# Kernel tuning notes

Measured on AMD Instinct MI355X. Metric: run time of the kernel, lower is better.

## Reference

```python
import jax, jax.numpy as jnp
import numpy as np

KS, KT = 3, 3  # Chebyshev order, temporal kernel


def _conv_t(x, w, b):
    # x: [B,C,T,N], w: [C_out,C_in,KT,1] -> valid conv over T
    y = jax.lax.conv_general_dilated(x, w, (1, 1), 'VALID',
                                     dimension_numbers=('NCHW', 'OIHW', 'NCHW'))
    return y + b[None, :, None, None]


def _glu_tconv(x, w, b, aw, ab):
    c_out = w.shape[0] // 2
    # Align (c_in > c_out): 1x1 conv, then crop first KT-1 steps
    x_in = (jnp.einsum('bctn,oc->botn', x, aw) + ab[None, :, None, None])[:, :, KT - 1:, :]
    xc = _conv_t(x, w, b)
    return (xc[:, :c_out] + x_in) * jax.nn.sigmoid(xc[:, c_out:])


def _relu_tconv(x, w, b):
    c_out = w.shape[0]
    pad = c_out - x.shape[1]
    # Align (c_in < c_out): zero-pad channels, then crop first KT-1 steps
    x_in = jnp.pad(x, ((0, 0), (0, pad), (0, 0), (0, 0)))[:, :, KT - 1:, :]
    return jax.nn.relu(_conv_t(x, w, b) + x_in)


def _sconv(x, basis, theta, bias):
    # Chebyshev graph conv: knm,bitm -> bitkn then channel mix iok,bitkn -> botn
    x_c = jnp.einsum('knm,bitm->bitkn', basis, x)
    x_gc = jnp.einsum('iok,bitkn->botn', theta, x_c) + bias[None, :, None, None]
    return jax.nn.relu(x_gc + x)  # align is identity (c_in == c_out)


def _layer_norm(x, g, b):
    # LayerNorm over [node_num, channels]: permute to [B,T,N,C], normalize last 2 dims
    y = jnp.transpose(x, (0, 2, 3, 1))
    mu = jnp.mean(y, axis=(-2, -1), keepdims=True)
    var = jnp.var(y, axis=(-2, -1), keepdims=True)
    y = (y - mu) * jax.lax.rsqrt(var + 1e-5) * g + b
    return jnp.transpose(y, (0, 3, 1, 2))


def _cheb_basis(graph):
    n = graph.shape[0]
    eye = jnp.eye(n, dtype=graph.dtype)
    g = graph + eye
    d = jnp.clip(jnp.sum(g, axis=-1), 1e-6, None) ** -0.5
    lap = eye - d[:, None] * g * d[None, :]
    cheb = [eye, lap]
    for _ in range(2, KS):
        cheb.append(2.0 * (lap @ cheb[-1]) - cheb[-2])
    return jnp.stack(cheb[:KS])


def _block(x, basis, t1_w, t1_b, t1_aw, t1_ab, s_theta, s_bias, t2_w, t2_b, ln_g, ln_b):
    x = _glu_tconv(x, t1_w, t1_b, t1_aw, t1_ab)
    x = _sconv(x, basis, s_theta, s_bias)
    x = _relu_tconv(x, t2_w, t2_b)
    return _layer_norm(x, ln_g, ln_b)  # dropout: eval mode (identity)


def setup_inputs() -> dict:
    B, N, T = 16, 2000, 12
    D_IN, D_OUT, C_MID = 3, 64, 32
    keys = jax.random.split(jax.random.key(0), 24)
    k = iter(range(24))

    def nrm(shape, scale=0.05):
        return jax.random.normal(keys[next(k)], shape, dtype=jnp.float32) * scale

    inp = {}
    inp['x'] = jax.random.normal(keys[next(k)], (B, D_IN, T, N), dtype=jnp.float32)
    inp['graph'] = jax.random.uniform(keys[next(k)], (N, N), dtype=jnp.float32)
    inp['in_w'] = nrm((D_IN, D_OUT), 0.3)
    inp['in_b'] = nrm((D_OUT,))
    for blk in ('b1', 'b2'):
        inp[blk + '_t1_w'] = nrm((2 * C_MID, D_OUT, KT, 1))
        inp[blk + '_t1_b'] = nrm((2 * C_MID,))
        inp[blk + '_t1_aw'] = nrm((C_MID, D_OUT))
        inp[blk + '_t1_ab'] = nrm((C_MID,))
        inp[blk + '_s_theta'] = nrm((C_MID, C_MID, KS))
        inp[blk + '_s_bias'] = nrm((C_MID,))
        inp[blk + '_t2_w'] = nrm((D_OUT, C_MID, KT, 1))
        inp[blk + '_t2_b'] = nrm((D_OUT,))
        inp[blk + '_ln_g'] = jnp.ones((N, D_OUT), dtype=jnp.float32)
        inp[blk + '_ln_b'] = jnp.zeros((N, D_OUT), dtype=jnp.float32)
    return inp


def reference(x, graph, in_w, in_b,
              b1_t1_w, b1_t1_b, b1_t1_aw, b1_t1_ab, b1_s_theta, b1_s_bias,
              b1_t2_w, b1_t2_b, b1_ln_g, b1_ln_b,
              b2_t1_w, b2_t1_b, b2_t1_aw, b2_t1_ab, b2_s_theta, b2_s_bias,
              b2_t2_w, b2_t2_b, b2_ln_g, b2_ln_b):
    # input_conv: 1x1 conv == channel matmul
    h = jnp.einsum('bctn,co->botn', x, in_w) + in_b[None, :, None, None]
    basis = _cheb_basis(graph)
    h = _block(h, basis, b1_t1_w, b1_t1_b, b1_t1_aw, b1_t1_ab,
               b1_s_theta, b1_s_bias, b1_t2_w, b1_t2_b, b1_ln_g, b1_ln_b)
    h = _block(h, basis, b2_t1_w, b2_t1_b, b2_t1_aw, b2_t1_ab,
               b2_s_theta, b2_s_bias, b2_t2_w, b2_t2_b, b2_ln_g, b2_ln_b)
    return h  # [B, 64, T-4*(KT-1)=4, N]
```

## Files before the change

### kernel.cpp

```cpp
#include <hip/hip_runtime.h>


typedef unsigned short u16;
typedef __attribute__((ext_vector_type(8))) short short8;
typedef __attribute__((ext_vector_type(4))) float floatx4;

struct __attribute__((aligned(8))) us4 { u16 v[4]; };

#define AS1 __attribute__((address_space(1)))
#define AS3 __attribute__((address_space(3)))

__device__ __forceinline__ float b2f(u16 h) {
  union { unsigned int u; float f; } v;
  v.u = ((unsigned int)h) << 16;
  return v.f;
}
__device__ __forceinline__ u16 f2b(float f) {
  union { float f; unsigned int u; } v;
  v.f = f;
  unsigned int r = (v.u + 0x7fffu + ((v.u >> 16) & 1u)) >> 16;
  return (u16)r;
}
__device__ __forceinline__ void gl_lds16(const u16* g, u16* l) {
  __builtin_amdgcn_global_load_lds((const AS1 unsigned int*)g,
                                   (AS3 unsigned int*)l, 16, 0, 0);
}
__device__ __forceinline__ us4 load4_guard(const u16* gp, int n) {
  if (n + 3 < 2000) return *(const us4*)gp;
  us4 r;
#pragma unroll
  for (int i = 0; i < 4; ++i) r.v[i] = (n + i < 2000) ? gp[i] : (u16)0;
  return r;
}


__global__ void k_deg(const float* __restrict__ graph, float* __restrict__ d) {
  const int n = blockIdx.x;
  const int tid = threadIdx.x;
  float s = 0.f;
  const float* row = graph + (size_t)n * 2000;
  for (int m4 = tid; m4 < 500; m4 += 256) {
    const float4 g = *(const float4*)(row + m4 * 4);
    s += (g.x + g.y) + (g.z + g.w);
  }
  __shared__ float red[256];
  red[tid] = s;
  __syncthreads();
  for (int st = 128; st > 0; st >>= 1) {
    if (tid < st) red[tid] += red[tid + st];
    __syncthreads();
  }
  if (tid == 0) d[n] = rsqrtf(fmaxf(red[0] + 1.f, 1e-6f));
}

__global__ void k_lap(const float* __restrict__ graph, const float* __restrict__ d,
                      u16* __restrict__ L) {
  const int m = blockIdx.x * 1024 + threadIdx.x * 4;
  const int n = blockIdx.y;
  us4 r = {{0, 0, 0, 0}};
  if (n < 2000 && m < 2000) {
    const float4 g4 = *(const float4*)(graph + (size_t)n * 2000 + m);
    const float4 d4 = *(const float4*)(d + m);
    const float dn = d[n];
    const float gv[4] = {g4.x, g4.y, g4.z, g4.w};
    const float dv[4] = {d4.x, d4.y, d4.z, d4.w};
#pragma unroll
    for (int i = 0; i < 4; ++i) {
      const float delta = (n == m + i) ? 1.f : 0.f;
      r.v[i] = f2b(delta - dn * (gv[i] + delta) * dv[i]);
    }
  }
  *(us4*)(L + (size_t)n * 2048 + m) = r;
}

__global__ __launch_bounds__(256, 4)
void k_inconv(const float* __restrict__ x, const float* __restrict__ w,
              const float* __restrict__ bias, u16* __restrict__ h0T) {
  const int n0 = blockIdx.x * 64;
  const int b = blockIdx.y / 12, t = blockIdx.y % 12;
  const int tid = threadIdx.x;
  u16* outb = h0T + ((size_t)(b * 12 + t) * 2048 + n0) * 64;
  const float* xb = x + ((size_t)(b * 3) * 12 + t) * 2000;
#pragma unroll
  for (int q = 0; q < 4; ++q) {
    const int f = q * 256 + tid;
    const int nl = f >> 4;
    const int c4 = (f & 15) * 4;
    const int n = n0 + nl;
    us4 r = {{0, 0, 0, 0}};
    if (n < 2000) {
      const float a0 = xb[n];
      const float a1 = xb[12 * 2000 + n];
      const float a2 = xb[2 * 12 * 2000 + n];
#pragma unroll
      for (int j = 0; j < 4; ++j) {
        const int o = c4 + j;
        r.v[j] = f2b(a0 * w[o] + a1 * w[64 + o] + a2 * w[128 + o] + bias[o]);
      }
    }
    *(us4*)(outb + f * 4) = r;
  }
}

__global__ void k_wpack(const float* __restrict__ t1w, const float* __restrict__ aw,
                        const float* __restrict__ th, const float* __restrict__ t2w,
                        u16* __restrict__ wglu, u16* __restrict__ wth,
                        u16* __restrict__ wt2) {
  const int mode = blockIdx.x;
  const int tid = threadIdx.x;
  if (mode == 0) {
    for (int idx = tid; idx < 1536 * 8; idx += 256) {
      int chunk = idx >> 3, j = idx & 7;
      int l15 = chunk & 15, quad = (chunk >> 4) & 3, g = chunk >> 6;
      int ks = g % 6, mi = g / 6;
      int o = mi * 16 + l15;
      int k = ks * 32 + quad * 8 + j;
      int c = k & 63, dt = k >> 6;
      float v = t1w[(o * 64 + c) * 3 + dt];
      if (o < 32 && dt == 2) v += aw[o * 64 + c];
      wglu[idx] = f2b(v);
    }
  } else if (mode == 1) {
    for (int idx = tid; idx < 512 * 8; idx += 256) {
      int chunk = idx >> 3, j = idx & 7;
      int l15 = chunk & 15, quad = (chunk >> 4) & 3, g = chunk >> 6;
      float v = 0.f;
      if (g < 6) {
        int ks = g % 3, mi = g / 3;
        int o = mi * 16 + l15;
        int k = ks * 32 + quad * 8 + j;
        int i = k & 31, src = k >> 5;
        const float* p = th + (i * 32 + o) * 3;
        v = (src == 0) ? (p[0] - p[2]) : (src == 1 ? p[1] : 2.f * p[2]);
      }
      wth[idx] = f2b(v);
    }
  } else {
    for (int idx = tid; idx < 768 * 8; idx += 256) {
      int chunk = idx >> 3, j = idx & 7;
      int l15 = chunk & 15, quad = (chunk >> 4) & 3, g = chunk >> 6;
      int ks = g % 3, mi = g / 3;
      int o = mi * 16 + l15;
      int k = ks * 32 + quad * 8 + j;
      int i = k & 31, dt = k >> 5;
      wt2[idx] = f2b(t2w[(o * 32 + i) * 3 + dt]);
    }
  }
}

__global__ __launch_bounds__(256, 4)
void k_mixT(const u16* __restrict__ xT, const u16* __restrict__ wp,
            const float* __restrict__ b0, const float* __restrict__ b1,
            u16* __restrict__ out, int T_in, int T, int tcnt) {
  __shared__ __align__(16) u16 lw[1536 * 8];
  __shared__ __align__(16) u16 lo[2][32][72];
  const int tid = threadIdx.x;
  const int lane = tid & 63, wave = tid >> 6;
  const int quad = lane >> 4, l15 = lane & 15;
  const int n0 = blockIdx.x * 64;
  const int b = blockIdx.y;
  const int t0 = blockIdx.z * tcnt;

#pragma unroll
  for (int p = 0; p < 6; ++p)
    gl_lds16(wp + (size_t)(p * 256 + wave * 64 + lane) * 8,
             &lw[(p * 256 + wave * 64) * 8]);

  float svb[8], gtb[8];
#pragma unroll
  for (int mi = 0; mi < 2; ++mi)
#pragma unroll
    for (int r = 0; r < 4; ++r) {
      const int i = mi * 16 + quad * 4 + r;
      svb[mi * 4 + r] = b0[i] + b1[i];
      gtb[mi * 4 + r] = b0[32 + i];
    }

  const int n = n0 + wave * 16 + l15;
  const size_t PL = (size_t)2048 * 64;
  const u16* px = xT + ((size_t)(b * T_in + t0) * 2048 + n) * 64 + quad * 8;

  short8 fa = *(const short8*)(px);
  short8 fb = *(const short8*)(px + 32);
  short8 fc = *(const short8*)(px + PL);
  short8 fd = *(const short8*)(px + PL + 32);

  const int rch = tid >> 3;
  const int rn8 = (tid & 7) * 8;

  asm volatile("s_waitcnt vmcnt(0)" ::: "memory");
  __syncthreads();

  for (int tt = 0; tt < tcnt; ++tt) {
    const int t = t0 + tt;
    const short8 fe = *(const short8*)(px + 2 * PL);
    const short8 ff = *(const short8*)(px + 2 * PL + 32);
    px += PL;

    floatx4 acc[4] = {};
    const short8 fr[6] = {fa, fb, fc, fd, fe, ff};
#pragma unroll
    for (int ks = 0; ks < 6; ++ks)
#pragma unroll
      for (int mi = 0; mi < 4; ++mi) {
        short8 afr = *(const short8*)&lw[((mi * 6 + ks) * 64 + lane) * 8];
        acc[mi] = __builtin_amdgcn_mfma_f32_16x16x32_bf16(afr, fr[ks], acc[mi], 0, 0, 0);
      }
    fa = fc; fb = fd; fc = fe; fd = ff;

    u16(*lob)[72] = lo[tt & 1];
#pragma unroll
    for (int mi = 0; mi < 2; ++mi)
#pragma unroll
      for (int r = 0; r < 4; ++r) {
        const int i = mi * 16 + quad * 4 + r;
        const float sv = acc[mi][r] + svb[mi * 4 + r];
        const float gt = acc[mi + 2][r] + gtb[mi * 4 + r];
        const float val = sv / (1.f + __expf(-gt));
        lob[i][wave * 16 + l15] = f2b(val);
      }
    __syncthreads();

    *(short8*)(out + (size_t)((b * 32 + rch) * T + t) * 2048 + n0 + rn8) =
        *(const short8*)&lob[rch][rn8];
  }
}

__global__ __launch_bounds__(256, 2)
void k_mix12(const u16* __restrict__ x0, const u16* __restrict__ y1,
             const u16* __restrict__ y2, const u16* __restrict__ wth,
             const u16* __restrict__ wt2, const float* __restrict__ sb,
             const float* __restrict__ t2b, u16* __restrict__ out,
             int T_g, int T_o) {
  __shared__ __align__(16) u16 lw1[512 * 8];
  __shared__ __align__(16) u16 lw2[768 * 8];
  __shared__ __align__(16) u16 lx[780 * 8];
  __shared__ __align__(16) u16 lt[10 * 260 * 8];

  const int tid = threadIdx.x;
  const int lane = tid & 63, wave = tid >> 6;
  const int quad = lane >> 4, l15 = lane & 15;
  const int n0 = blockIdx.x * 64;
  const int b = blockIdx.y;
  const int n = n0 + wave * 16 + l15;

#pragma unroll
  for (int p = 0; p < 2; ++p)
    gl_lds16(wth + (size_t)(p * 256 + wave * 64 + lane) * 8,
             &lw1[(p * 256 + wave * 64) * 8]);
#pragma unroll
  for (int p = 0; p < 3; ++p)
    gl_lds16(wt2 + (size_t)(p * 256 + wave * 64 + lane) * 8,
             &lw2[(p * 256 + wave * 64) * 8]);

  const int nloc = (tid & 15) * 4;
  const int g16 = tid >> 4;

  for (int t = 0; t < T_g; ++t) {
    __syncthreads();
    us4 rv[2][4];
#pragma unroll
    for (int p = 0; p < 2; ++p) {
      const int k4 = p * 16 + g16;
      if (k4 < 24) {
#pragma unroll
        for (int i = 0; i < 4; ++i) {
          const int k = k4 * 4 + i;
          const u16* base = (k < 32) ? x0 : ((k < 64) ? y1 : y2);
          rv[p][i] = *(const us4*)(base +
              (size_t)((b * 32 + (k & 31)) * T_g + t) * 2048 + n0 + nloc);
        }
      }
    }
#pragma unroll
    for (int p = 0; p < 2; ++p) {
      const int k4 = p * 16 + g16;
      if (k4 < 24) {
        const int ks = k4 >> 3, q8 = k4 & 7;
        const int quadw = (q8 >> 1) & 3;
        const int j0 = (q8 & 1) * 4;
#pragma unroll
        for (int i = 0; i < 4; ++i) {
          const int nn = nloc + i;
          const int chunk = (ks * 4 + (nn >> 4)) * 65 + quadw * 16 + (nn & 15);
          us4 wv;
          wv.v[0] = rv[p][0].v[i]; wv.v[1] = rv[p][1].v[i];
          wv.v[2] = rv[p][2].v[i]; wv.v[3] = rv[p][3].v[i];
          *(us4*)&lx[chunk * 8 + j0] = wv;
        }
      }
    }
    __syncthreads();

    floatx4 acc[2] = {};
#pragma unroll
    for (int ks = 0; ks < 3; ++ks) {
      short8 bfr = *(const short8*)&lx[((ks * 4 + wave) * 65 + lane) * 8];
#pragma unroll
      for (int mi = 0; mi < 2; ++mi) {
        short8 afr = *(const short8*)&lw1[((mi * 3 + ks) * 64 + lane) * 8];
        acc[mi] = __builtin_amdgcn_mfma_f32_16x16x32_bf16(afr, bfr, acc[mi], 0, 0, 0);
      }
    }
#pragma unroll
    for (int mi = 0; mi < 2; ++mi)
#pragma unroll
      for (int r = 0; r < 4; ++r) {
        const int o = mi * 16 + quad * 4 + r;
        const float v = acc[mi][r] + sb[o] +
            b2f(lx[(wave * 65 + ((o >> 3) & 3) * 16 + l15) * 8 + (o & 7)]);
        lt[((t * 4 + wave) * 65 + ((o >> 3) & 3) * 16 + l15) * 8 + (o & 7)] =
            f2b(fmaxf(v, 0.f));
      }
  }
  __syncthreads();

  for (int to = 0; to < T_o; ++to) {
    floatx4 acc[4] = {};
#pragma unroll
    for (int ks = 0; ks < 3; ++ks) {
      short8 bfr = *(const short8*)&lt[(((to + ks) * 4 + wave) * 65 + lane) * 8];
#pragma unroll
      for (int mi = 0; mi < 4; ++mi) {
        short8 afr = *(const short8*)&lw2[((mi * 3 + ks) * 64 + lane) * 8];
        acc[mi] = __builtin_amdgcn_mfma_f32_16x16x32_bf16(afr, bfr, acc[mi], 0, 0, 0);
      }
    }
    if (n < 2000) {
#pragma unroll
      for (int mi = 0; mi < 4; ++mi)
#pragma unroll
        for (int r = 0; r < 4; ++r) {
          const int o = mi * 16 + quad * 4 + r;
          float v = acc[mi][r] + t2b[o];
          if (o < 32)
            v += b2f(lt[(((to + 2) * 4 + wave) * 65 +
                         ((o >> 3) & 3) * 16 + l15) * 8 + (o & 7)]);
          out[(size_t)((b * 64 + o) * T_o + to) * 2000 + n] = f2b(fmaxf(v, 0.f));
        }
    }
  }
}

template <int BM, int MPAD, int DPW>
__global__ __launch_bounds__(512, 1)
void k_gemm(const u16* __restrict__ A, const u16* __restrict__ Bt,
            u16* __restrict__ C) {
  constexpr int K = 2048;
  constexpr int NTI = K / 64;
  constexpr int AFR = BM / 32;
  constexpr int WM = BM / 2;
  constexpr int S1 = (AFR + 1) / 2;
  constexpr int C1 = DPW - 4;
  constexpr int BROWS = 512;
  constexpr int ROWS = BROWS + 2 * MPAD;
  __shared__ __align__(16) u16 lds[2][ROWS * 32];

  const int tid = threadIdx.x;
  const int lane = tid & 63, wave = tid >> 6;
  const int quad = lane >> 4, l15 = lane & 15;
  const int m0 = blockIdx.y * BM, n0 = blockIdx.x * 256;
  const int wy = wave >> 2, wx = wave & 3;

  const int lr = lane >> 2;
  const int qv = (((lane & 3) - (lr + (lr >> 2))) & 3);
  const u16* sp[DPW];
  int dofs[DPW];
#pragma unroll
  for (int d = 0; d < DPW; ++d) {
    const int f = wave * DPW + d;
    if (f < 32) {
      const int rb = f >> 1, ks = f & 1;
      sp[d] = Bt + (size_t)(n0 + rb * 16 + lr) * K + ks * 32 + qv * 8;
      dofs[d] = (ks * 256 + rb * 16) * 32;
    } else {
      const int g = f - 32;
      const int rb = g >> 1, ks = g & 1;
      sp[d] = A + (size_t)(m0 + rb * 16 + lr) * K + ks * 32 + qv * 8;
      dofs[d] = (BROWS + ks * MPAD + rb * 16) * 32;
    }
  }

  const int sigr = (l15 + (l15 >> 2)) & 3;
  const int cofs = ((quad + sigr) & 3) * 8;

  floatx4 acc[AFR][4] = {};

#pragma unroll
  for (int d = 0; d < DPW; ++d) gl_lds16(sp[d], &lds[0][dofs[d]]);
#pragma unroll
  for (int d = 0; d < C1; ++d) gl_lds16(sp[d] + 64, &lds[1][dofs[d]]);
  if constexpr (C1 == 3) asm volatile("s_waitcnt vmcnt(3)" ::: "memory");
  else                   asm volatile("s_waitcnt vmcnt(2)" ::: "memory");
  asm volatile("s_barrier" ::: "memory");

  for (int it = 0; it < NTI; ++it) {
    const u16* cb = lds[it & 1];
    u16* nb = lds[(it & 1) ^ 1];
    u16* pb = lds[it & 1];
    const int kn1 = (it + 1) * 64;
    const bool st1 = (it + 1 < NTI);
    short8 bf[4], af[AFR];

#pragma unroll
    for (int ni = 0; ni < 4; ++ni)
      bf[ni] = *(const short8*)&cb[(wx * 64 + ni * 16 + l15) * 32 + cofs];
#pragma unroll
    for (int mi = 0; mi < S1; ++mi)
      af[mi] = *(const short8*)&cb[(BROWS + wy * WM + mi * 16 + l15) * 32 + cofs];
    if (st1) {
      gl_lds16(sp[C1] + kn1, &nb[dofs[C1]]);
      gl_lds16(sp[C1 + 1] + kn1, &nb[dofs[C1 + 1]]);
    }
#pragma unroll
    for (int mi = 0; mi < S1; ++mi)
#pragma unroll
      for (int ni = 0; ni < 4; ++ni)
        acc[mi][ni] = __builtin_amdgcn_mfma_f32_16x16x32_bf16(
            af[mi], bf[ni], acc[mi][ni], 0, 0, 0);

#pragma unroll
    for (int mi = S1; mi < AFR; ++mi)
      af[mi] = *(const short8*)&cb[(BROWS + wy * WM + mi * 16 + l15) * 32 + cofs];
    if (st1) {
      gl_lds16(sp[C1 + 2] + kn1, &nb[dofs[C1 + 2]]);
      gl_lds16(sp[C1 + 3] + kn1, &nb[dofs[C1 + 3]]);
    }
#pragma unroll
    for (int mi = S1; mi < AFR; ++mi)
#pragma unroll
      for (int ni = 0; ni < 4; ++ni)
        acc[mi][ni] = __builtin_amdgcn_mfma_f32_16x16x32_bf16(
            af[mi], bf[ni], acc[mi][ni], 0, 0, 0);

#pragma unroll
    for (int ni = 0; ni < 4; ++ni)
      bf[ni] = *(const short8*)&cb[(256 + wx * 64 + ni * 16 + l15) * 32 + cofs];
#pragma unroll
    for (int mi = 0; mi < S1; ++mi)
      af[mi] = *(const short8*)&cb[(BROWS + MPAD + wy * WM + mi * 16 + l15) * 32 + cofs];
#pragma unroll
    for (int mi = 0; mi < S1; ++mi)
#pragma unroll
      for (int ni = 0; ni < 4; ++ni)
        acc[mi][ni] = __builtin_amdgcn_mfma_f32_16x16x32_bf16(
            af[mi], bf[ni], acc[mi][ni], 0, 0, 0);

#pragma unroll
    for (int mi = S1; mi < AFR; ++mi)
      af[mi] = *(const short8*)&cb[(BROWS + MPAD + wy * WM + mi * 16 + l15) * 32 + cofs];
#pragma unroll
    for (int mi = S1; mi < AFR; ++mi)
#pragma unroll
      for (int ni = 0; ni < 4; ++ni)
        acc[mi][ni] = __builtin_amdgcn_mfma_f32_16x16x32_bf16(
            af[mi], bf[ni], acc[mi][ni], 0, 0, 0);

    asm volatile("s_waitcnt lgkmcnt(0)" ::: "memory");
    asm volatile("s_barrier" ::: "memory");
    if (it + 2 < NTI) {
      const int kn2 = (it + 2) * 64;
#pragma unroll
      for (int d = 0; d < C1; ++d) gl_lds16(sp[d] + kn2, &pb[dofs[d]]);
      if constexpr (C1 == 3) asm volatile("s_waitcnt vmcnt(3)" ::: "memory");
      else                   asm volatile("s_waitcnt vmcnt(2)" ::: "memory");
    } else {
      asm volatile("s_waitcnt vmcnt(0)" ::: "memory");
    }
    asm volatile("s_barrier" ::: "memory");
  }

#pragma unroll
  for (int mi = 0; mi < AFR; ++mi) {
#pragma unroll
    for (int ni = 0; ni < 4; ++ni) {
      const int row = m0 + wy * WM + mi * 16 + quad * 4;
      const int col = n0 + wx * 64 + ni * 16 + l15;
#pragma unroll
      for (int r = 0; r < 4; ++r)
        C[(size_t)(row + r) * K + col] = f2b(acc[mi][ni][r]);
    }
  }
}


__global__ void k_lnpart(const u16* __restrict__ h, float* __restrict__ part, int T) {
  const int bt = blockIdx.x, cg = blockIdx.y;
  const int b = bt / T, t = bt % T;
  const int tid = threadIdx.x;
  float s = 0.f, ss = 0.f;
  for (int c = cg * 8; c < cg * 8 + 8; ++c) {
    const u16* row = h + (size_t)((b * 64 + c) * T + t) * 2000;
    for (int n = tid * 4; n < 2000; n += 1024) {
      const us4 hv = *(const us4*)(row + n);
#pragma unroll
      for (int i = 0; i < 4; ++i) {
        const float v = b2f(hv.v[i]);
        s += v; ss += v * v;
      }
    }
  }
  __shared__ float r1[256], r2[256];
  r1[tid] = s; r2[tid] = ss;
  __syncthreads();
  for (int st = 128; st > 0; st >>= 1) {
    if (tid < st) { r1[tid] += r1[tid + st]; r2[tid] += r2[tid + st]; }
    __syncthreads();
  }
  if (tid == 0) {
    part[(bt * 8 + cg) * 2 + 0] = r1[0];
    part[(bt * 8 + cg) * 2 + 1] = r2[0];
  }
}

__global__ void k_lnfin(const float* __restrict__ part, float* __restrict__ stats,
                        int BT) {
  const int i = blockIdx.x * 256 + threadIdx.x;
  if (i >= BT) return;
  float s = 0.f, ss = 0.f;
  for (int g = 0; g < 8; ++g) {
    s  += part[(i * 8 + g) * 2 + 0];
    ss += part[(i * 8 + g) * 2 + 1];
  }
  const float inv = 1.f / 128000.f;
  const float mu = s * inv;
  const float var = ss * inv - mu * mu;
  stats[i * 2] = mu;
  stats[i * 2 + 1] = rsqrtf(var + 1e-5f);
}

__global__ __launch_bounds__(256, 4)
void k_lnapT(const u16* __restrict__ h, const float* __restrict__ stats,
             const float* __restrict__ gw, const float* __restrict__ gb,
             u16* __restrict__ hT, int T) {
  __shared__ u16 tile[64][72];
  const int tid = threadIdx.x;
  const int n0 = blockIdx.x * 64;
  const int bt = blockIdx.y;
  const int b = bt / T, t = bt % T;
  const float mu = stats[bt * 2], rs = stats[bt * 2 + 1];

  {
    const int c = tid >> 2;
    const int nq = (tid & 3) * 16;
    const u16* row = h + (size_t)((b * 64 + c) * T + t) * 2000 + n0 + nq;
#pragma unroll
    for (int k = 0; k < 4; ++k) {
      const us4 v = load4_guard(row + k * 4, n0 + nq + k * 4);
      *(us4*)&tile[c][nq + k * 4] = v;
    }
  }
  __syncthreads();

  const int n = tid >> 2;
  const int c0 = (tid & 3) * 16;
  const int gn = n0 + n;
  u16* dst = hT + ((size_t)(b * T + t) * 2048 + gn) * 64 + c0;
  if (gn >= 2000) {
    const us4 z = {{0, 0, 0, 0}};
#pragma unroll
    for (int q = 0; q < 4; ++q) *(us4*)(dst + q * 4) = z;
    return;
  }
#pragma unroll
  for (int q = 0; q < 4; ++q) {
    us4 r;
#pragma unroll
    for (int j = 0; j < 4; ++j) {
      const int cc = c0 + q * 4 + j;
      const float gv = gw[(size_t)gn * 64 + cc];
      const float bv = gb[(size_t)gn * 64 + cc];
      r.v[j] = f2b((b2f(tile[cc][n]) - mu) * rs * gv + bv);
    }
    *(us4*)(dst + q * 4) = r;
  }
}

__global__ void k_lngbT(const float* __restrict__ gw, const float* __restrict__ gb,
                        float* __restrict__ gwT, float* __restrict__ gbT) {
  const int n = blockIdx.x * 256 + threadIdx.x;
  const int c = blockIdx.y;
  float vw = 0.f, vb = 0.f;
  if (n < 2000) {
    vw = gw[(size_t)n * 64 + c];
    vb = gb[(size_t)n * 64 + c];
  }
  gwT[(size_t)c * 2048 + n] = vw;
  gbT[(size_t)c * 2048 + n] = vb;
}

__global__ void k_lnapply(const u16* __restrict__ h, const float* __restrict__ stats,
                          const float* __restrict__ gwT, const float* __restrict__ gbT,
                          float* __restrict__ outf, int T) {
  const int n = blockIdx.x * 1024 + threadIdx.x * 4;
  if (n >= 2000) return;
  int by = blockIdx.y;
  const int t = by % T; by /= T;
  const int c = by & 63;
  const int b = by >> 6;
  const int bt = b * T + t;
  const float mu = stats[bt * 2], rs = stats[bt * 2 + 1];
  const size_t row = (size_t)((b * 64 + c) * T + t) * 2000 + n;
  const us4 hv = *(const us4*)(h + row);
  const float4 w4 = *(const float4*)(gwT + (size_t)c * 2048 + n);
  const float4 b4 = *(const float4*)(gbT + (size_t)c * 2048 + n);
  const float o0 = (b2f(hv.v[0]) - mu) * rs * w4.x + b4.x;
  const float o1 = (b2f(hv.v[1]) - mu) * rs * w4.y + b4.y;
  const float o2 = (b2f(hv.v[2]) - mu) * rs * w4.z + b4.z;
  const float o3 = (b2f(hv.v[3]) - mu) * rs * w4.w + b4.w;
  *(float4*)(outf + row) = make_float4(o0, o1, o2, o3);
}


extern "C" void kernel_launch(void* const* d_in, const int* in_sizes, int n_in,
                              void* d_out, int out_size, void* d_ws, size_t ws_size,
                              hipStream_t stream) {
  const float* x     = (const float*)d_in[0];
  const float* graph = (const float*)d_in[1];
  const float* in_w  = (const float*)d_in[2];
  const float* in_b  = (const float*)d_in[3];

  char* ws = (char*)d_ws;
  size_t off = 0;
  auto alloc = [&](size_t bytes) -> void* {
    void* p = ws + off;
    off += (bytes + 255) & ~(size_t)255;
    return p;
  };
  float* dd    = (float*)alloc(2048 * 4);
  float* stats = (float*)alloc(16 * 12 * 2 * 4);
  float* part  = (float*)alloc(16 * 8 * 8 * 2 * 4);
  float* gwT   = (float*)alloc((size_t)64 * 2048 * 4);
  float* gbT   = (float*)alloc((size_t)64 * 2048 * 4);
  u16* wpg  = (u16*)alloc((size_t)1536 * 8 * 2);
  u16* wpt  = (u16*)alloc((size_t)512 * 8 * 2);
  u16* wp2  = (u16*)alloc((size_t)768 * 8 * 2);
  u16* L    = (u16*)alloc((size_t)2048 * 2048 * 2);
  u16* h0T  = (u16*)alloc((size_t)16 * 12 * 2048 * 64 * 2);
  u16* Xp   = (u16*)alloc((size_t)5120 * 2048 * 2);
  u16* Y1   = (u16*)alloc((size_t)5120 * 2048 * 2);
  u16* Y2   = (u16*)alloc((size_t)5120 * 2048 * 2);
  u16* h1   = (u16*)alloc((size_t)16 * 64 * 8 * 2000 * 2);
  u16* h1T  = h0T;
  if (off > ws_size) return;

  k_deg<<<dim3(2000), dim3(256), 0, stream>>>(graph, dd);
  k_lap<<<dim3(2, 2048), dim3(256), 0, stream>>>(graph, dd, L);
  k_inconv<<<dim3(32, 192), dim3(256), 0, stream>>>(x, in_w, in_b, h0T);

  for (int blk = 0; blk < 2; ++blk) {
    const int base = 4 + blk * 10;
    const float* t1w = (const float*)d_in[base + 0];
    const float* t1b = (const float*)d_in[base + 1];
    const float* aw  = (const float*)d_in[base + 2];
    const float* ab  = (const float*)d_in[base + 3];
    const float* th  = (const float*)d_in[base + 4];
    const float* sb  = (const float*)d_in[base + 5];
    const float* t2w = (const float*)d_in[base + 6];
    const float* t2b = (const float*)d_in[base + 7];
    const float* lng = (const float*)d_in[base + 8];
    const float* lnb = (const float*)d_in[base + 9];

    const int T_in = (blk == 0) ? 12 : 8;
    const int T_g  = T_in - 2;
    const int T_o  = T_g - 2;
    const u16* hinT = (blk == 0) ? h0T : h1T;

    k_wpack<<<dim3(3), dim3(256), 0, stream>>>(t1w, aw, th, t2w, wpg, wpt, wp2);
    k_mixT<<<dim3(32, 16, 2), dim3(256), 0, stream>>>(
        hinT, wpg, t1b, ab, Xp, T_in, T_g, T_g / 2);
    if (blk == 0) {
      k_gemm<160, 192, 7><<<dim3(8, 32), dim3(512), 0, stream>>>(Xp, L, Y1);
      k_gemm<160, 192, 7><<<dim3(8, 32), dim3(512), 0, stream>>>(Y1, L, Y2);
    } else {
      k_gemm<96, 128, 6><<<dim3(8, 32), dim3(512), 0, stream>>>(Xp, L, Y1);
      k_gemm<96, 128, 6><<<dim3(8, 32), dim3(512), 0, stream>>>(Y1, L, Y2);
    }
    k_mix12<<<dim3(32, 16), dim3(256), 0, stream>>>(
        Xp, Y1, Y2, wpt, wp2, sb, t2b, h1, T_g, T_o);
    k_lnpart<<<dim3(16 * T_o, 8), dim3(256), 0, stream>>>(h1, part, T_o);
    k_lnfin<<<dim3(1), dim3(256), 0, stream>>>(part, stats, 16 * T_o);
    if (blk == 0) {
      k_lnapT<<<dim3(32, 16 * T_o), dim3(256), 0, stream>>>(
          h1, stats, lng, lnb, h1T, T_o);
    } else {
      k_lngbT<<<dim3(8, 64), dim3(256), 0, stream>>>(lng, lnb, gwT, gbT);
      k_lnapply<<<dim3(2, 16 * 64 * T_o), dim3(256), 0, stream>>>(
          h1, stats, gwT, gbT, (float*)d_out, T_o);
    }
  }
}
```

Measured before the change: 442.1 us.

## Fuse LayerNorm partial statistics into mix12 epilogue with atomics and staged stores

The LayerNorm sum and sum-of-squares reduction moves into the k_mix12 epilogue. Each block reduces its values with wave shuffles and atomically adds them into a per-(b,t) buffer, which k_wpack zeroes. This removes the separate k_lnpart kernel, its launch, and the re-read of h1. The output tile is also staged through LDS so it can be written with 16-byte vector stores instead of scattered 2-byte stores. In exchange it adds two barriers per time step, global float atomics, and summation order that is no longer deterministic.

```diff
diff --git a/kernel.cpp b/kernel.cpp
--- a/kernel.cpp
+++ b/kernel.cpp
@@ -105,7 +105,7 @@
 __global__ void k_wpack(const float* __restrict__ t1w, const float* __restrict__ aw,
                         const float* __restrict__ th, const float* __restrict__ t2w,
                         u16* __restrict__ wglu, u16* __restrict__ wth,
-                        u16* __restrict__ wt2) {
+                        u16* __restrict__ wt2, float* __restrict__ part2) {
   const int mode = blockIdx.x;
   const int tid = threadIdx.x;
   if (mode == 0) {
@@ -121,6 +121,7 @@
       wglu[idx] = f2b(v);
     }
   } else if (mode == 1) {
+    part2[tid] = 0.f;
     for (int idx = tid; idx < 512 * 8; idx += 256) {
       int chunk = idx >> 3, j = idx & 7;
       int l15 = chunk & 15, quad = (chunk >> 4) & 3, g = chunk >> 6;
@@ -231,11 +232,12 @@
              const u16* __restrict__ y2, const u16* __restrict__ wth,
              const u16* __restrict__ wt2, const float* __restrict__ sb,
              const float* __restrict__ t2b, u16* __restrict__ out,
-             int T_g, int T_o) {
+             float* __restrict__ part2, int T_g, int T_o) {
   __shared__ __align__(16) u16 lw1[512 * 8];
   __shared__ __align__(16) u16 lw2[768 * 8];
   __shared__ __align__(16) u16 lx[780 * 8];
   __shared__ __align__(16) u16 lt[10 * 260 * 8];
+  __shared__ float red[8];
 
   const int tid = threadIdx.x;
   const int lane = tid & 63, wave = tid >> 6;
@@ -315,6 +317,7 @@
   }
   __syncthreads();
 
+  u16(*lo)[72] = (u16(*)[72])lx;
   for (int to = 0; to < T_o; ++to) {
     floatx4 acc[4] = {};
 #pragma unroll
@@ -326,18 +329,45 @@
         acc[mi] = __builtin_amdgcn_mfma_f32_16x16x32_bf16(afr, bfr, acc[mi], 0, 0, 0);
       }
     }
-    if (n < 2000) {
-#pragma unroll
-      for (int mi = 0; mi < 4; ++mi)
-#pragma unroll
-        for (int r = 0; r < 4; ++r) {
-          const int o = mi * 16 + quad * 4 + r;
-          float v = acc[mi][r] + t2b[o];
-          if (o < 32)
-            v += b2f(lt[(((to + 2) * 4 + wave) * 65 +
-                         ((o >> 3) & 3) * 16 + l15) * 8 + (o & 7)]);
-          out[(size_t)((b * 64 + o) * T_o + to) * 2000 + n] = f2b(fmaxf(v, 0.f));
+    float s = 0.f, ss = 0.f;
+#pragma unroll
+    for (int mi = 0; mi < 4; ++mi)
+#pragma unroll
+      for (int r = 0; r < 4; ++r) {
+        const int o = mi * 16 + quad * 4 + r;
+        float v = acc[mi][r] + t2b[o];
+        if (o < 32)
+          v += b2f(lt[(((to + 2) * 4 + wave) * 65 +
+                       ((o >> 3) & 3) * 16 + l15) * 8 + (o & 7)]);
+        const u16 hv = f2b(fmaxf(v, 0.f));
+        lo[o][wave * 16 + l15] = hv;
+        if (n < 2000) {
+          const float vq = b2f(hv);
+          s += vq; ss += vq * vq;
         }
+      }
+    __syncthreads();
+
+#pragma unroll
+    for (int q = 0; q < 2; ++q) {
+      const int f = q * 256 + tid;
+      const int ch = f >> 3;
+      const int n8 = (f & 7) * 8;
+      if (n0 + n8 < 2000)
+        *(short8*)(out + (size_t)((b * 64 + ch) * T_o + to) * 2000 + n0 + n8) =
+            *(const short8*)&lo[ch][n8];
+    }
+
+#pragma unroll
+    for (int off = 32; off > 0; off >>= 1) {
+      s += __shfl_down(s, off);
+      ss += __shfl_down(ss, off);
+    }
+    if (lane == 0) { red[wave * 2] = s; red[wave * 2 + 1] = ss; }
+    __syncthreads();
+    if (tid == 0) {
+      atomicAdd(&part2[(b * T_o + to) * 2 + 0], red[0] + red[2] + red[4] + red[6]);
+      atomicAdd(&part2[(b * T_o + to) * 2 + 1], red[1] + red[3] + red[5] + red[7]);
     }
   }
 }
@@ -484,47 +514,13 @@
 }
 
 
-__global__ void k_lnpart(const u16* __restrict__ h, float* __restrict__ part, int T) {
-  const int bt = blockIdx.x, cg = blockIdx.y;
-  const int b = bt / T, t = bt % T;
-  const int tid = threadIdx.x;
-  float s = 0.f, ss = 0.f;
-  for (int c = cg * 8; c < cg * 8 + 8; ++c) {
-    const u16* row = h + (size_t)((b * 64 + c) * T + t) * 2000;
-    for (int n = tid * 4; n < 2000; n += 1024) {
-      const us4 hv = *(const us4*)(row + n);
-#pragma unroll
-      for (int i = 0; i < 4; ++i) {
-        const float v = b2f(hv.v[i]);
-        s += v; ss += v * v;
-      }
-    }
-  }
-  __shared__ float r1[256], r2[256];
-  r1[tid] = s; r2[tid] = ss;
-  __syncthreads();
-  for (int st = 128; st > 0; st >>= 1) {
-    if (tid < st) { r1[tid] += r1[tid + st]; r2[tid] += r2[tid + st]; }
-    __syncthreads();
-  }
-  if (tid == 0) {
-    part[(bt * 8 + cg) * 2 + 0] = r1[0];
-    part[(bt * 8 + cg) * 2 + 1] = r2[0];
-  }
-}
-
-__global__ void k_lnfin(const float* __restrict__ part, float* __restrict__ stats,
+__global__ void k_lnfin(const float* __restrict__ part2, float* __restrict__ stats,
                         int BT) {
   const int i = blockIdx.x * 256 + threadIdx.x;
   if (i >= BT) return;
-  float s = 0.f, ss = 0.f;
-  for (int g = 0; g < 8; ++g) {
-    s  += part[(i * 8 + g) * 2 + 0];
-    ss += part[(i * 8 + g) * 2 + 1];
-  }
   const float inv = 1.f / 128000.f;
-  const float mu = s * inv;
-  const float var = ss * inv - mu * mu;
+  const float mu = part2[i * 2] * inv;
+  const float var = part2[i * 2 + 1] * inv - mu * mu;
   stats[i * 2] = mu;
   stats[i * 2 + 1] = rsqrtf(var + 1e-5f);
 }
@@ -629,7 +625,7 @@
   };
   float* dd    = (float*)alloc(2048 * 4);
   float* stats = (float*)alloc(16 * 12 * 2 * 4);
-  float* part  = (float*)alloc(16 * 8 * 8 * 2 * 4);
+  float* part2 = (float*)alloc(256 * 4);
   float* gwT   = (float*)alloc((size_t)64 * 2048 * 4);
   float* gbT   = (float*)alloc((size_t)64 * 2048 * 4);
   u16* wpg  = (u16*)alloc((size_t)1536 * 8 * 2);
@@ -666,7 +662,8 @@
     const int T_o  = T_g - 2;
     const u16* hinT = (blk == 0) ? h0T : h1T;
 
-    k_wpack<<<dim3(3), dim3(256), 0, stream>>>(t1w, aw, th, t2w, wpg, wpt, wp2);
+    k_wpack<<<dim3(3), dim3(256), 0, stream>>>(t1w, aw, th, t2w, wpg, wpt, wp2,
+                                               part2);
     k_mixT<<<dim3(32, 16, 2), dim3(256), 0, stream>>>(
         hinT, wpg, t1b, ab, Xp, T_in, T_g, T_g / 2);
     if (blk == 0) {
@@ -677,9 +674,8 @@
       k_gemm<96, 128, 6><<<dim3(8, 32), dim3(512), 0, stream>>>(Y1, L, Y2);
     }
     k_mix12<<<dim3(32, 16), dim3(256), 0, stream>>>(
-        Xp, Y1, Y2, wpt, wp2, sb, t2b, h1, T_g, T_o);
-    k_lnpart<<<dim3(16 * T_o, 8), dim3(256), 0, stream>>>(h1, part, T_o);
-    k_lnfin<<<dim3(1), dim3(256), 0, stream>>>(part, stats, 16 * T_o);
+        Xp, Y1, Y2, wpt, wp2, sb, t2b, h1, part2, T_g, T_o);
+    k_lnfin<<<dim3(1), dim3(256), 0, stream>>>(part2, stats, 16 * T_o);
     if (blk == 0) {
       k_lnapT<<<dim3(32, 16 * T_o), dim3(256), 0, stream>>>(
           h1, stats, lng, lnb, h1T, T_o);
```

Result: slower. 452.3 us (+2.3%).
